# Kernel tuning notes

Hardware: AMD Instinct MI355X
Metric: run time of the kernel (lower is better)

Reference implementation:

```python
import jax, jax.numpy as jnp
import numpy as np

B, C1, C2, N1, N2 = 8, 16, 32, 256, 128


def _masks():
    # static numpy masks, mirroring EquivariantLayer.__init__
    n_max, n_min = max(N1, N2), min(N1, N2)
    k = np.arange(n_max)
    k[k > n_max // 2] -= n_max
    mask = np.abs(k) <= n_min / 2            # |k| <= n_min/2 (both nyquists)
    mask2 = mask[: n_max // 2 + 1].copy()    # taken BEFORE removing neg nyquist
    nyq_pos = k == n_min / 2
    nyq_pos2 = nyq_pos[: n_max // 2 + 1]
    nyq_neg = k == -n_min / 2
    mask[nyq_neg] = False                    # drop negative nyquist row
    return mask, mask2, nyq_pos, nyq_pos2

MASK, MASK2, NYQ_POS, NYQ_POS2 = _masks()


def rot90_kernel(t):
    # 90-deg rotation about grid point [0,0] for periodic kernels:
    # transpose last two dims, keep column 0, reverse remaining columns
    t = jnp.swapaxes(t, -1, -2)
    return jnp.concatenate([t[..., :1], t[..., 1:][..., ::-1]], axis=-1)


def symmetric_kernel(kernel):
    # average over the 8 elements of D4 (rotations + transpose*rotations)
    k1 = kernel
    k2 = rot90_kernel(k1)
    k3 = rot90_kernel(k2)
    k4 = rot90_kernel(k3)
    k5 = jnp.swapaxes(k1, -1, -2)
    k6 = rot90_kernel(k5)
    k7 = rot90_kernel(k6)
    k8 = rot90_kernel(k7)
    return (k1 + k2 + k3 + k4 + k5 + k6 + k7 + k8) / 8.0


def _forward(f, kernel):
    F = jnp.fft.rfft2(f)                                  # [b,c1,N1,N1//2+1]
    # downsample: zero nyquist modes, truncate spectrum, rescale
    F = jnp.where(jnp.asarray(NYQ_POS)[None, None, :, None], 0, F)
    F = jnp.where(jnp.asarray(NYQ_POS2)[None, None, None, :], 0, F)
    F = F[:, :, MASK, :][:, :, :, MASK2] * (N2 / N1) ** 2  # [b,c1,N2,N2//2+1]
    # spectral convolution with D4-symmetrized kernel
    K = jnp.fft.rfft2(symmetric_kernel(kernel))            # [1,c1,c2,N2,N2//2+1]
    conv = jnp.einsum('bcnk,cdnk->bdnk', F, K[0])          # sum over input channels
    return jnp.fft.irfft2(F), jnp.fft.irfft2(conv)


def setup_inputs() -> dict:
    key = jax.random.key(0)
    kf, kk = jax.random.split(key)
    f = jax.random.normal(kf, (B, C1, N1, N1), dtype=jnp.float32)
    eps = 0.1
    kernel = eps * (2.0 * jax.random.uniform(kk, (1, C1, C2, N2, N2), dtype=jnp.float32) - 1.0)
    return {"f": f, "kernel": kernel}


def reference(f, kernel):
    return _forward(f, kernel)
```

## Files before the change

### kernel.cpp

```cpp
#include <hip/hip_runtime.h>

#define PI_F 3.14159265358979f

typedef unsigned int  uint32;
typedef unsigned short ushort16;

__device__ __forceinline__ float2 cmul(float2 a, float2 b) {
    return make_float2(a.x * b.x - a.y * b.y, a.x * b.y + a.y * b.x);
}
__device__ __forceinline__ float2 cadd(float2 a, float2 b) { return make_float2(a.x + b.x, a.y + b.y); }
__device__ __forceinline__ float2 csub(float2 a, float2 b) { return make_float2(a.x - b.x, a.y - b.y); }
__device__ __forceinline__ float2 shflx(float2 v, int m) {
    return make_float2(__shfl_xor(v.x, m, 64), __shfl_xor(v.y, m, 64));
}
__device__ __forceinline__ float2 shfli(float2 v, int src) {
    return make_float2(__shfl(v.x, src, 64), __shfl(v.y, src, 64));
}
__device__ __forceinline__ int brev6(int x) { return (int)(__brev((unsigned)x) >> 26); }

__device__ __forceinline__ uint32 bfu(float x) {
    uint32 u = __float_as_uint(x);
    return (u + 0x7FFFu + ((u >> 16) & 1u)) >> 16;
}
__device__ __forceinline__ uint32 packbf2(float2 v) { return bfu(v.x) | (bfu(v.y) << 16); }
__device__ __forceinline__ float2 unpackbf2(uint32 u) {
    return make_float2(__uint_as_float(u << 16), __uint_as_float(u & 0xFFFF0000u));
}
__device__ __forceinline__ float bf2f(ushort16 u) { return __uint_as_float((uint32)u << 16); }

template<int CTRL>
__device__ __forceinline__ float dpp1(float x) {
    return __builtin_bit_cast(float, __builtin_amdgcn_update_dpp(
        0, __builtin_bit_cast(int, x), CTRL, 0xF, 0xF, true));
}
template<int CTRL>
__device__ __forceinline__ float2 dppx(float2 v) {
    return make_float2(dpp1<CTRL>(v.x), dpp1<CTRL>(v.y));
}
template<int M>
__device__ __forceinline__ float2 xorx(float2 v) {
    if constexpr (M == 1)      return dppx<0xB1>(v);
    else if constexpr (M == 2) return dppx<0x4E>(v);
    else if constexpr (M == 8) return dppx<0x128>(v);
    else                       return shflx(v, M);
}

template<bool INV>
__device__ __forceinline__ void tw_init(int lane, float2* w, float* sg) {
#pragma unroll
    for (int t = 0; t < 6; ++t) {
        int m = 32 >> t;
        bool up = (lane & m) != 0;
        int pos = lane & (m - 1);
        float ang = (INV ? PI_F : -PI_F) * (float)pos / (float)m;
        float sn, cs;
        __sincosf(ang, &sn, &cs);
        w[t]  = up ? make_float2(cs, sn) : make_float2(1.f, 0.f);
        sg[t] = up ? -1.f : 1.f;
    }
}

__device__ __forceinline__ float2 fft64s(float2 v, const float2* w, const float* sg) {
#define FFT_STAGE(T, M) { float2 p = xorx<M>(v);                                   \
        float2 d = make_float2(fmaf(sg[T], v.x, p.x), fmaf(sg[T], v.y, p.y));      \
        v = cmul(d, w[T]); }
    FFT_STAGE(0, 32) FFT_STAGE(1, 16) FFT_STAGE(2, 8)
    FFT_STAGE(3, 4)  FFT_STAGE(4, 2)  FFT_STAGE(5, 1)
#undef FFT_STAGE
    return v;
}

__device__ void kfft_body(const float* __restrict__ kin, ushort16* __restrict__ kout,
                          float2* X, int img) {
    int lane = threadIdx.x & 63, wv = threadIdx.x >> 6;
    float2 w[6]; float sg[6];
    tw_init<false>(lane, w, sg);
    int b6 = brev6(lane);
    float sn, cs;
    __sincosf(-PI_F * (float)lane * (1.0f / 64.0f), &sn, &cs);
    float2 w64 = make_float2(cs, sn);
    __sincosf(-PI_F * (float)b6 * (1.0f / 64.0f), &sn, &cs);
    float2 wub = make_float2(cs, sn);
    const float2* in2 = (const float2*)(kin + (size_t)img * 16384);
    int gm2 = brev6((64 - b6) & 63);
#pragma unroll 2
    for (int rr = 0; rr < 16; ++rr) {
        int r = wv * 16 + rr;
        float2 z = in2[r * 64 + lane];
        z = fft64s(z, w, sg);
        float2 zm = shfli(z, gm2);
        float ar = z.x + zm.x, ai = z.y - zm.y;
        float br = z.x - zm.x, bi = z.y + zm.y;
        float p = wub.x * br - wub.y * bi, q = wub.x * bi + wub.y * br;
        X[r * 65 + b6] = make_float2(0.5f * (ar + q), 0.5f * (ai - p));
    }
    __syncthreads();
    float2 c0[8], c1[8];
#pragma unroll
    for (int cc = 0; cc < 8; ++cc) {
        int k = wv * 8 + cc;
        c0[cc] = X[lane * 65 + k];
        c1[cc] = X[(lane + 64) * 65 + k];
    }
    __syncthreads();
    float* Rr = (float*)X;
#pragma unroll
    for (int cc = 0; cc < 8; ++cc) {
        int k = wv * 8 + cc;
        float2 r0 = c0[cc], r1 = c1[cc];
        float2 t = r0;
        r0 = cadd(t, r1);
        r1 = cmul(csub(t, r1), w64);
        r0 = fft64s(r0, w, sg);
        r1 = fft64s(r1, w, sg);
        Rr[(2 * b6) * 65 + k]     = r0.x;
        Rr[(2 * b6 + 1) * 65 + k] = r1.x;
    }
    __syncthreads();
    ushort4* ko4 = (ushort4*)(kout + (size_t)img * 8192);
    for (int i = threadIdx.x; i < 2048; i += 512) {
        int n = i >> 4, k4 = (i & 15) << 2;
        float op[4];
#pragma unroll
        for (int m = 0; m < 4; ++m) {
            int k = k4 + m;
            float t1 = Rr[n * 65 + k];
            float t2 = Rr[((128 - n) & 127) * 65 + k];
            float t3, t4;
            if (n < 64) {
                t3 = Rr[k * 65 + n];
                t4 = Rr[((128 - k) & 127) * 65 + n];
            } else {
                int c2 = 128 - n; if (c2 > 63) c2 = 63;
                t3 = Rr[((128 - k) & 127) * 65 + c2];
                t4 = Rr[k * 65 + c2];
            }
            op[m] = 0.25f * (t1 + t2 + t3 + t4);
        }
        ushort4 o4;
        o4.x = (ushort16)bfu(op[0]); o4.y = (ushort16)bfu(op[1]);
        o4.z = (ushort16)bfu(op[2]); o4.w = (ushort16)bfu(op[3]);
        ko4[i] = o4;
    }
}

__device__ void rfft_body(const float* __restrict__ f, uint32* __restrict__ G, int bid) {
    int lane = threadIdx.x & 63, wv = threadIdx.x >> 6;
    int row0 = (bid * 8 + wv) * 8;
    float2 w[6]; float sg[6];
    tw_init<false>(lane, w, sg);
    int m = brev6(lane);
    float sn, cs;
    __sincosf(-PI_F * (float)lane * (1.0f / 64.0f), &sn, &cs);
    float2 w64 = make_float2(cs, sn);
    __sincosf(-PI_F * (float)(2 * m) * (1.0f / 128.0f), &sn, &cs);
    float2 wue = make_float2(cs, sn);
    __sincosf(-PI_F * (float)(2 * m + 1) * (1.0f / 128.0f), &sn, &cs);
    float2 wuo = make_float2(cs, sn);
    int src_e = brev6((64 - m) & 63);
    int src_o = brev6(63 - m);
    bool active = (lane & 1) == 0;
#pragma unroll 2
    for (int rr = 0; rr < 8; ++rr) {
        size_t row = (size_t)(row0 + rr);
        const float2* x = (const float2*)(f + row * 256);
        float2 r0 = x[lane], r1 = x[lane + 64];
        float2 t = r0;
        r0 = cadd(t, r1);
        r1 = cmul(csub(t, r1), w64);
        r0 = fft64s(r0, w, sg);
        r1 = fft64s(r1, w, sg);
        float2 zme = shfli(r0, src_e);
        float2 zmo = shfli(r1, src_o);
        float ar = r0.x + zme.x, ai = r0.y - zme.y;
        float br = r0.x - zme.x, bi = r0.y + zme.y;
        float p = wue.x * br - wue.y * bi, q = wue.x * bi + wue.y * br;
        uint32 xe = packbf2(make_float2(0.5f * (ar + q), 0.5f * (ai - p)));
        ar = r1.x + zmo.x; ai = r1.y - zmo.y;
        br = r1.x - zmo.x; bi = r1.y + zmo.y;
        p = wuo.x * br - wuo.y * bi; q = wuo.x * bi + wuo.y * br;
        uint32 xo = packbf2(make_float2(0.5f * (ar + q), 0.5f * (ai - p)));
        if (active) ((uint2*)(G + row * 64))[m] = make_uint2(xe, xo);
    }
}

__global__ __launch_bounds__(512) void mega_a(const float* __restrict__ kin,
                                              ushort16* __restrict__ Kr,
                                              const float* __restrict__ f,
                                              uint32* __restrict__ G) {
    __shared__ float2 SH[128 * 65];
    int bid = blockIdx.x;
    if (bid < 512) kfft_body(kin, Kr, SH, bid);
    else           rfft_body(f, G, bid - 512);
}

__global__ __launch_bounds__(512) void fcolk(const uint32* __restrict__ G,
                                             uint32* __restrict__ FH) {
    __shared__ uint32 S[256 * 17];
    int img = blockIdx.x >> 2, qg = blockIdx.x & 3;
    int lane = threadIdx.x & 63, wv = threadIdx.x >> 6;
    float2 w[6]; float sg[6];
    tw_init<false>(lane, w, sg);
    float sn, cs;
    __sincosf(-PI_F * (float)lane * (1.0f / 64.0f), &sn, &cs);
    float2 w64 = make_float2(cs, sn);
    __sincosf(-PI_F * (float)lane * (1.0f / 128.0f), &sn, &cs);
    float2 w128a = make_float2(cs, sn);
    __sincosf(-PI_F * (float)(lane + 64) * (1.0f / 128.0f), &sn, &cs);
    float2 w128b = make_float2(cs, sn);
    const uint32* src = G + (size_t)img * 16384 + qg * 16;
    for (int i = threadIdx.x; i < 4096; i += 512) {
        int r = i >> 4, c = i & 15;
        S[r * 17 + c] = src[(size_t)r * 64 + c];
    }
    __syncthreads();
    float2 q0[2], q1[2], q2[2], q3[2];
#pragma unroll
    for (int cc = 0; cc < 2; ++cc) {
        int c = wv * 2 + cc;
        q0[cc] = unpackbf2(S[(lane)       * 17 + c]);
        q1[cc] = unpackbf2(S[(lane +  64) * 17 + c]);
        q2[cc] = unpackbf2(S[(lane + 128) * 17 + c]);
        q3[cc] = unpackbf2(S[(lane + 192) * 17 + c]);
    }
    __syncthreads();
    int b6 = brev6(lane);
#pragma unroll
    for (int cc = 0; cc < 2; ++cc) {
        int c = wv * 2 + cc;
        float2 r0 = q0[cc], r1 = q1[cc], r2 = q2[cc], r3 = q3[cc], t;
        t = r0; r0 = cadd(t, r2); r2 = cmul(csub(t, r2), w128a);
        t = r1; r1 = cadd(t, r3); r3 = cmul(csub(t, r3), w128b);
        t = r0; r0 = cadd(t, r1); r1 = cmul(csub(t, r1), w64);
        t = r2; r2 = cadd(t, r3); r3 = cmul(csub(t, r3), w64);
        r0 = fft64s(r0, w, sg); r1 = fft64s(r1, w, sg);
        r2 = fft64s(r2, w, sg); r3 = fft64s(r3, w, sg);
        float2 vv[4] = { r0, r2, r1, r3 };
#pragma unroll
        for (int j = 0; j < 4; ++j) {
            int n = 4 * b6 + j;
            int r = (n < 64) ? n : ((n >= 193) ? n - 128 : -1);
            if (r >= 0)
                S[r * 17 + c] = packbf2(make_float2(vv[j].x * 0.25f, vv[j].y * 0.25f));
        }
    }
    __syncthreads();
    uint32* dst = FH + (size_t)img * 8192 + qg * 16;
    for (int i = threadIdx.x; i < 2048; i += 512) {
        int r = i >> 4, c = i & 15;
        dst[(size_t)r * 64 + c] = (r == 64) ? 0u : S[r * 17 + c];
    }
}

__device__ void einsum_body(const uint32* __restrict__ F, const ushort16* __restrict__ K,
                            uint32* __restrict__ C, uint32* Ft, int bid) {
    int nk0 = bid * 32;
    int t = threadIdx.x;
    for (int i = t; i < 4096; i += 512) {
        int bc = i >> 5, nl = i & 31;
        Ft[i] = F[(size_t)bc * 8192 + nk0 + nl];
    }
    __syncthreads();
    int nl = t & 31, dg = t >> 5;
    int nk = nk0 + nl;
    float2 acc[2][8] = {};
#pragma unroll
    for (int c = 0; c < 16; ++c) {
        float2 fv[8];
#pragma unroll
        for (int b = 0; b < 8; ++b) fv[b] = unpackbf2(Ft[(b * 16 + c) * 32 + nl]);
#pragma unroll
        for (int j = 0; j < 2; ++j) {
            int d = j * 16 + dg;
            float kv = bf2f(K[(size_t)(c * 32 + d) * 8192 + nk]);
#pragma unroll
            for (int b = 0; b < 8; ++b) {
                acc[j][b].x = fmaf(fv[b].x, kv, acc[j][b].x);
                acc[j][b].y = fmaf(fv[b].y, kv, acc[j][b].y);
            }
        }
    }
#pragma unroll
    for (int j = 0; j < 2; ++j) {
        int d = j * 16 + dg;
#pragma unroll
        for (int b = 0; b < 8; ++b)
            C[(size_t)(b * 32 + d) * 8192 + nk] = packbf2(acc[j][b]);
    }
}

__device__ void ifuse_body(const uint32* __restrict__ src, float2* __restrict__ dst,
                           float2* S) {
    int lane = threadIdx.x & 63, wv = threadIdx.x >> 6;
    float2 w[6]; float sg[6];
    tw_init<true>(lane, w, sg);
    float sn, cs;
    __sincosf(PI_F * (float)lane * (1.0f / 64.0f), &sn, &cs);
    float2 w64 = make_float2(cs, sn);
    for (int i = threadIdx.x; i < 8192; i += 512) {
        int r = i >> 6, c = i & 63;
        S[r * 65 + c] = unpackbf2(src[i]);
    }
    __syncthreads();
    float2 c0[8], c1[8];
#pragma unroll
    for (int cc = 0; cc < 8; ++cc) {
        int k = wv * 8 + cc;
        c0[cc] = S[lane * 65 + k];
        c1[cc] = S[(lane + 64) * 65 + k];
    }
    __syncthreads();
    int b6 = brev6(lane);
#pragma unroll
    for (int cc = 0; cc < 8; ++cc) {
        int k = wv * 8 + cc;
        float2 r0 = c0[cc], r1 = c1[cc];
        float2 t = r0;
        r0 = cadd(t, r1);
        r1 = cmul(csub(t, r1), w64);
        r0 = fft64s(r0, w, sg);
        r1 = fft64s(r1, w, sg);
        S[(2 * b6) * 65 + k]     = r0;
        S[(2 * b6 + 1) * 65 + k] = r1;
    }
    __syncthreads();
#pragma unroll 2
    for (int rr = 0; rr < 16; ++rr) {
        int m = wv * 16 + rr;
        float2 X = S[m * 65 + lane];
        float2 Xm = shfli(X, (64 - lane) & 63);
        if (lane == 0) Xm = make_float2(0.f, 0.f);
        float er = 0.5f * (X.x + Xm.x), ei = 0.5f * (X.y - Xm.y);
        float br = 0.5f * (X.x - Xm.x), bi = 0.5f * (X.y + Xm.y);
        float orr = w64.x * br - w64.y * bi, oi = w64.x * bi + w64.y * br;
        float2 Z = make_float2(er - oi, ei + orr);
        Z = fft64s(Z, w, sg);
        dst[m * 64 + b6] = make_float2(Z.x * (1.0f / 8192.0f), Z.y * (1.0f / 8192.0f));
    }
}

__global__ __launch_bounds__(512) void mega2(const uint32* __restrict__ FH,
                                             const ushort16* __restrict__ Kr,
                                             uint32* __restrict__ CONV,
                                             float* __restrict__ out) {
    __shared__ float2 SH[128 * 65];
    int bid = blockIdx.x;
    if (bid < 256) einsum_body(FH, Kr, CONV, (uint32*)SH, bid);
    else {
        int img = bid - 256;
        ifuse_body(FH + (size_t)img * 8192, (float2*)(out + (size_t)img * 16384), SH);
    }
}

__global__ __launch_bounds__(512) void ifuse1(const uint32* __restrict__ CV,
                                              float* __restrict__ out1) {
    __shared__ float2 SH[128 * 65];
    int img = blockIdx.x;
    ifuse_body(CV + (size_t)img * 8192, (float2*)(out1 + (size_t)img * 16384), SH);
}

extern "C" void kernel_launch(void* const* d_in, const int* in_sizes, int n_in,
                              void* d_out, int out_size, void* d_ws, size_t ws_size,
                              hipStream_t stream) {
    const float* f   = (const float*)d_in[0];
    const float* kin = (const float*)d_in[1];
    float* out = (float*)d_out;
    char* ws = (char*)d_ws;

    uint32*   G    = (uint32*)ws;
    uint32*   CONV = (uint32*)ws;
    uint32*   FHAT = (uint32*)(ws + 8388608);
    ushort16* Kr   = (ushort16*)(ws + 16777216);

    mega_a<<<1024, 512, 0, stream>>>(kin, Kr, f, G);
    fcolk<<<512, 512, 0, stream>>>(G, FHAT);
    mega2<<<384, 512, 0, stream>>>(FHAT, Kr, CONV, out);
    ifuse1<<<256, 512, 0, stream>>>(CONV, out + 2097152);
}
```

Baseline: 159.6 us.

## Fuse row and column FFT of input into one per-image kernel

```diff
diff --git a/kernel.cpp b/kernel.cpp
--- a/kernel.cpp
+++ b/kernel.cpp
@@ -144,9 +144,9 @@
     }
 }
 
-__device__ void rfft_body(const float* __restrict__ f, uint32* __restrict__ G, int bid) {
+__device__ void ffull_body(const float* __restrict__ f, uint32* __restrict__ FH,
+                           uint32* A, int img) {
     int lane = threadIdx.x & 63, wv = threadIdx.x >> 6;
-    int row0 = (bid * 8 + wv) * 8;
     float2 w[6]; float sg[6];
     tw_init<false>(lane, w, sg);
     int m = brev6(lane);
@@ -160,11 +160,11 @@
     int src_e = brev6((64 - m) & 63);
     int src_o = brev6(63 - m);
     bool active = (lane & 1) == 0;
+    const float2* base = (const float2*)(f + (size_t)img * 65536);
 #pragma unroll 2
-    for (int rr = 0; rr < 8; ++rr) {
-        size_t row = (size_t)(row0 + rr);
-        const float2* x = (const float2*)(f + row * 256);
-        float2 r0 = x[lane], r1 = x[lane + 64];
+    for (int rr = 0; rr < 32; ++rr) {
+        int r = wv * 32 + rr;
+        float2 r0 = base[r * 128 + lane], r1 = base[r * 128 + 64 + lane];
         float2 t = r0;
         r0 = cadd(t, r1);
         r1 = cmul(csub(t, r1), w64);
@@ -180,55 +180,25 @@
         br = r1.x - zmo.x; bi = r1.y + zmo.y;
         p = wuo.x * br - wuo.y * bi; q = wuo.x * bi + wuo.y * br;
         uint32 xo = packbf2(make_float2(0.5f * (ar + q), 0.5f * (ai - p)));
-        if (active) ((uint2*)(G + row * 64))[m] = make_uint2(xe, xo);
-    }
-}
-
-__global__ __launch_bounds__(512) void mega_a(const float* __restrict__ kin,
-                                              ushort16* __restrict__ Kr,
-                                              const float* __restrict__ f,
-                                              uint32* __restrict__ G) {
-    __shared__ float2 SH[128 * 65];
-    int bid = blockIdx.x;
-    if (bid < 512) kfft_body(kin, Kr, SH, bid);
-    else           rfft_body(f, G, bid - 512);
-}
-
-__global__ __launch_bounds__(512) void fcolk(const uint32* __restrict__ G,
-                                             uint32* __restrict__ FH) {
-    __shared__ uint32 S[256 * 17];
-    int img = blockIdx.x >> 2, qg = blockIdx.x & 3;
-    int lane = threadIdx.x & 63, wv = threadIdx.x >> 6;
-    float2 w[6]; float sg[6];
-    tw_init<false>(lane, w, sg);
-    float sn, cs;
-    __sincosf(-PI_F * (float)lane * (1.0f / 64.0f), &sn, &cs);
-    float2 w64 = make_float2(cs, sn);
+        if (active) {
+            A[r * 65 + 2 * m]     = xe;
+            A[r * 65 + 2 * m + 1] = xo;
+        }
+    }
+    __syncthreads();
     __sincosf(-PI_F * (float)lane * (1.0f / 128.0f), &sn, &cs);
     float2 w128a = make_float2(cs, sn);
     __sincosf(-PI_F * (float)(lane + 64) * (1.0f / 128.0f), &sn, &cs);
     float2 w128b = make_float2(cs, sn);
-    const uint32* src = G + (size_t)img * 16384 + qg * 16;
-    for (int i = threadIdx.x; i < 4096; i += 512) {
-        int r = i >> 4, c = i & 15;
-        S[r * 17 + c] = src[(size_t)r * 64 + c];
-    }
-    __syncthreads();
-    float2 q0[2], q1[2], q2[2], q3[2];
-#pragma unroll
-    for (int cc = 0; cc < 2; ++cc) {
-        int c = wv * 2 + cc;
-        q0[cc] = unpackbf2(S[(lane)       * 17 + c]);
-        q1[cc] = unpackbf2(S[(lane +  64) * 17 + c]);
-        q2[cc] = unpackbf2(S[(lane + 128) * 17 + c]);
-        q3[cc] = unpackbf2(S[(lane + 192) * 17 + c]);
-    }
-    __syncthreads();
     int b6 = brev6(lane);
 #pragma unroll
-    for (int cc = 0; cc < 2; ++cc) {
-        int c = wv * 2 + cc;
-        float2 r0 = q0[cc], r1 = q1[cc], r2 = q2[cc], r3 = q3[cc], t;
+    for (int cc = 0; cc < 8; ++cc) {
+        int c = wv * 8 + cc;
+        float2 r0 = unpackbf2(A[(lane)       * 65 + c]);
+        float2 r1 = unpackbf2(A[(lane +  64) * 65 + c]);
+        float2 r2 = unpackbf2(A[(lane + 128) * 65 + c]);
+        float2 r3 = unpackbf2(A[(lane + 192) * 65 + c]);
+        float2 t;
         t = r0; r0 = cadd(t, r2); r2 = cmul(csub(t, r2), w128a);
         t = r1; r1 = cadd(t, r3); r3 = cmul(csub(t, r3), w128b);
         t = r0; r0 = cadd(t, r1); r1 = cmul(csub(t, r1), w64);
@@ -241,15 +211,25 @@
             int n = 4 * b6 + j;
             int r = (n < 64) ? n : ((n >= 193) ? n - 128 : -1);
             if (r >= 0)
-                S[r * 17 + c] = packbf2(make_float2(vv[j].x * 0.25f, vv[j].y * 0.25f));
+                A[r * 65 + c] = packbf2(make_float2(vv[j].x * 0.25f, vv[j].y * 0.25f));
         }
     }
     __syncthreads();
-    uint32* dst = FH + (size_t)img * 8192 + qg * 16;
-    for (int i = threadIdx.x; i < 2048; i += 512) {
-        int r = i >> 4, c = i & 15;
-        dst[(size_t)r * 64 + c] = (r == 64) ? 0u : S[r * 17 + c];
-    }
+    uint32* dst = FH + (size_t)img * 8192;
+    for (int i = threadIdx.x; i < 8192; i += 512) {
+        int r = i >> 6, c = i & 63;
+        dst[i] = (r == 64) ? 0u : A[r * 65 + c];
+    }
+}
+
+__global__ __launch_bounds__(512) void mega1(const float* __restrict__ kin,
+                                             ushort16* __restrict__ Kr,
+                                             const float* __restrict__ f,
+                                             uint32* __restrict__ FH) {
+    __shared__ uint32 SH[128 * 2 * 65];
+    int bid = blockIdx.x;
+    if (bid < 128) ffull_body(f, FH, SH, bid);
+    else           kfft_body(kin, Kr, (float2*)SH, bid - 128);
 }
 
 __device__ void einsum_body(const uint32* __restrict__ F, const ushort16* __restrict__ K,
@@ -367,13 +347,11 @@
     float* out = (float*)d_out;
     char* ws = (char*)d_ws;
 
-    uint32*   G    = (uint32*)ws;
     uint32*   CONV = (uint32*)ws;
     uint32*   FHAT = (uint32*)(ws + 8388608);
     ushort16* Kr   = (ushort16*)(ws + 16777216);
 
-    mega_a<<<1024, 512, 0, stream>>>(kin, Kr, f, G);
-    fcolk<<<512, 512, 0, stream>>>(G, FHAT);
+    mega1<<<640, 512, 0, stream>>>(kin, Kr, f, FHAT);
     mega2<<<384, 512, 0, stream>>>(FHAT, Kr, CONV, out);
     ifuse1<<<256, 512, 0, stream>>>(CONV, out + 2097152);
 }
```

New measurement: 165.1 us. 1.03x slower.
